# Optimization experiments

Hardware: AMD Instinct MI355X
Metric: run time of the kernel (lower is better)

## Reference

```python
import jax, jax.numpy as jnp
import numpy as np

EMBED = 512
HEADS = 8
HEAD_DIM = EMBED // HEADS


def setup_inputs() -> dict:
    key = jax.random.key(0)
    ks = jax.random.split(key, 11)
    B, S, E = 2, 4096, EMBED
    scale = 1.0 / np.sqrt(E)
    inp = {
        "q": jax.random.normal(ks[0], (B, S, E), dtype=jnp.float32),
        "k": jax.random.normal(ks[1], (B, S, E), dtype=jnp.float32),
        "v": jax.random.normal(ks[2], (B, S, E), dtype=jnp.float32),
        # linear layer params (torch nn.Linear: y = x @ W.T + b)
        "Wq": jax.random.normal(ks[3], (E, E), dtype=jnp.float32) * scale,
        "bq": jnp.zeros((E,), dtype=jnp.float32),
        "Wk": jax.random.normal(ks[4], (E, E), dtype=jnp.float32) * scale,
        "bk": jnp.zeros((E,), dtype=jnp.float32),
        "Wv": jax.random.normal(ks[5], (E, E), dtype=jnp.float32) * scale,
        "bv": jnp.zeros((E,), dtype=jnp.float32),
        "Wo": jax.random.normal(ks[6], (E, E), dtype=jnp.float32) * scale,
        "bo": jnp.zeros((E,), dtype=jnp.float32),
    }
    return inp


def reference(q, k, v, Wq, bq, Wk, bk, Wv, bv, Wo, bo):
    B, Sq, E = q.shape
    Sk = k.shape[1]
    H, D = HEADS, HEAD_DIM
    # projections, split heads: [B, S, H, D]
    qh = (q @ Wq.T + bq).reshape(B, Sq, H, D)
    kh = (k @ Wk.T + bk).reshape(B, Sk, H, D)
    vh = (v @ Wv.T + bv).reshape(B, Sk, H, D)
    # full score matrix [B, H, Sq, Sk]; note: scaled by sqrt(embed_size), matching source
    scores = jnp.einsum('bqhe,bkhe->bhqk', qh, kh) / jnp.sqrt(jnp.float32(E))
    probs = jax.nn.softmax(scores, axis=-1)
    attn = jnp.einsum('bhql,blhd->bqhd', probs, vh)  # [B, Sq, H, D]
    concat = attn.reshape(B, Sq, E)
    return concat @ Wo.T + bo
```

## Files before the change

kernel.cpp:

```cpp
#include <hip/hip_runtime.h>
#include <hip/hip_bf16.h>

#define DEVFN __device__ __forceinline__

typedef __attribute__((ext_vector_type(8))) __bf16 bf16x8;
typedef __attribute__((ext_vector_type(4))) float f32x4;
typedef __attribute__((ext_vector_type(16))) float f32x16;

constexpr int E  = 512;
constexpr int S  = 4096;
constexpr int HD = 64;
constexpr int RT = 8192;

DEVFN unsigned int cvt_pk_bf16(float lo, float hi) {
  unsigned int r;
  asm("v_cvt_pk_bf16_f32 %0, %1, %2" : "=v"(r) : "v"(lo), "v"(hi));
  return r;
}
DEVFN void plswap(unsigned int& a, unsigned int& b) {
  asm("v_permlane32_swap_b32 %0, %1" : "+v"(a), "+v"(b));
}
DEVFN float ex2(float x) { return __builtin_amdgcn_exp2f(x); }

DEVFN unsigned short f2bf(float f) {
  union { float f; unsigned int u; } v; v.f = f;
  unsigned int u = v.u;
  return (unsigned short)((u + 0x7fffu + ((u >> 16) & 1u)) >> 16);
}

DEVFN f32x4 mfma16(bf16x8 a, bf16x8 b, f32x4 c) {
  return __builtin_amdgcn_mfma_f32_16x16x32_bf16(a, b, c, 0, 0, 0);
}
DEVFN f32x16 mfma32(bf16x8 a, bf16x8 b, f32x16 c) {
  return __builtin_amdgcn_mfma_f32_32x32x16_bf16(a, b, c, 0, 0, 0);
}

DEVFN uint4 pk8(const float4& a, const float4& b) {
  uint4 r;
  r.x = cvt_pk_bf16(a.x, a.y); r.y = cvt_pk_bf16(a.z, a.w);
  r.z = cvt_pk_bf16(b.x, b.y); r.w = cvt_pk_bf16(b.z, b.w);
  return r;
}
DEVFN bf16x8 asbf(uint4 u) { union { uint4 a; bf16x8 b; } c; c.a = u; return c.b; }

template<typename TIN, int OMODE>
DEVFN void gemm_body(const TIN* __restrict__ X, const float* __restrict__ W,
                     const float* __restrict__ bias, void* __restrict__ outp,
                     float scale, unsigned short (*Al)[72], unsigned short (*Bl)[72]) {
  const int bid = blockIdx.x;
  const int bm = bid >> 2, bn = bid & 3;
  const int tid = threadIdx.x;
  const int w = tid >> 6, lane = tid & 63;
  const int g = lane >> 4, ln = lane & 15;
  const int wm = w >> 2, wn = w & 3;
  const int r0 = bm * 128, n0 = bn * 128;
  const int srw = tid >> 2, sc0 = (tid & 3) * 16;

  f32x4 acc[4][2] = {};

  float4 af[4];
  uint4  au[2];
  float4 bp[4];

  auto loadA = [&](int k0) {
    if constexpr (sizeof(TIN) == 4) {
      const float* src = (const float*)X + (size_t)(r0 + srw) * E + k0 + sc0;
      #pragma unroll
      for (int i = 0; i < 4; ++i) af[i] = *(const float4*)(src + i * 4);
    } else {
      const unsigned short* src = (const unsigned short*)X + (size_t)(r0 + srw) * E + k0 + sc0;
      #pragma unroll
      for (int i = 0; i < 2; ++i) au[i] = *(const uint4*)(src + i * 8);
    }
  };
  auto loadB = [&](int k0) {
    const float* src = W + (size_t)(n0 + srw) * E + k0 + sc0;
    #pragma unroll
    for (int i = 0; i < 4; ++i) bp[i] = *(const float4*)(src + i * 4);
  };

  loadA(0); loadB(0);

  for (int k0 = 0; k0 < E; k0 += 64) {
    if constexpr (sizeof(TIN) == 4) {
      *(uint4*)&Al[srw][sc0]     = pk8(af[0], af[1]);
      *(uint4*)&Al[srw][sc0 + 8] = pk8(af[2], af[3]);
    } else {
      *(uint4*)&Al[srw][sc0]     = au[0];
      *(uint4*)&Al[srw][sc0 + 8] = au[1];
    }
    *(uint4*)&Bl[srw][sc0]     = pk8(bp[0], bp[1]);
    *(uint4*)&Bl[srw][sc0 + 8] = pk8(bp[2], bp[3]);
    __syncthreads();
    if (k0 + 64 < E) { loadA(k0 + 64); loadB(k0 + 64); }

    __builtin_amdgcn_s_setprio(1);
    #pragma unroll
    for (int kk = 0; kk < 2; ++kk) {
      bf16x8 afr[4], bfr[2];
      #pragma unroll
      for (int i = 0; i < 4; ++i)
        afr[i] = *(const bf16x8*)&Al[wm*64 + i*16 + ln][kk*32 + 8*g];
      #pragma unroll
      for (int j = 0; j < 2; ++j)
        bfr[j] = *(const bf16x8*)&Bl[wn*32 + j*16 + ln][kk*32 + 8*g];
      #pragma unroll
      for (int i = 0; i < 4; ++i)
        #pragma unroll
        for (int j = 0; j < 2; ++j)
          acc[i][j] = mfma16(afr[i], bfr[j], acc[i][j]);
    }
    __builtin_amdgcn_s_setprio(0);
    __syncthreads();
  }

  #pragma unroll
  for (int j = 0; j < 2; ++j) {
    const int gcol = n0 + wn*32 + j*16 + ln;
    const float bv = bias[gcol];
    #pragma unroll
    for (int i = 0; i < 4; ++i) {
      const int gr = r0 + wm*64 + i*16 + 4*g;
      #pragma unroll
      for (int r = 0; r < 4; ++r) {
        const float v = (acc[i][j][r] + bv) * scale;
        if constexpr (OMODE == 1)
          ((float*)outp)[(size_t)(gr + r) * E + gcol] = v;
        else if constexpr (OMODE == 0)
          ((unsigned short*)outp)[(size_t)(gr + r) * E + gcol] = f2bf(v);
        else
          ((unsigned short*)outp)[((size_t)((gr + r) >> 12) * E + gcol) * S + ((gr + r) & (S - 1))] = f2bf(v);
      }
    }
  }
}

__global__ __launch_bounds__(512) void gemm_qkv(const float* __restrict__ q,
    const float* __restrict__ k, const float* __restrict__ v,
    const float* __restrict__ Wq, const float* __restrict__ bq,
    const float* __restrict__ Wk, const float* __restrict__ bk,
    const float* __restrict__ Wv, const float* __restrict__ bv,
    unsigned short* qh, unsigned short* kh, unsigned short* vhT, float qscale) {
  __shared__ unsigned short Al[128][72];
  __shared__ unsigned short Bl[128][72];
  const int y = blockIdx.y;
  if (y == 0)      gemm_body<float, 0>(q, Wq, bq, qh, qscale, Al, Bl);
  else if (y == 1) gemm_body<float, 0>(k, Wk, bk, kh, 1.0f, Al, Bl);
  else             gemm_body<float, 2>(v, Wv, bv, vhT, 1.0f, Al, Bl);
}

__global__ __launch_bounds__(512) void gemm_o(const unsigned short* __restrict__ cc,
    const float* __restrict__ Wo, const float* __restrict__ bo, float* out) {
  __shared__ unsigned short Al[128][72];
  __shared__ unsigned short Bl[128][72];
  gemm_body<unsigned short, 1>(cc, Wo, bo, out, 1.0f, Al, Bl);
}

__global__ __launch_bounds__(256) void attn_fwd(const unsigned short* __restrict__ qh,
                                                const unsigned short* __restrict__ kh,
                                                const unsigned short* __restrict__ vhT,
                                                unsigned short* __restrict__ cc) {
  __shared__ unsigned short K_lds[64][72];
  __shared__ unsigned short V_lds[64][72];

  const int bid = blockIdx.x;
  const int swz = (bid & 7) * 64 + (bid >> 3);
  const int bh = swz >> 5, qt = swz & 31;
  const int b = bh >> 3, h = bh & 7;

  const int tid = threadIdx.x;
  const int w = tid >> 6, lane = tid & 63;
  const int l31 = lane & 31, hi = lane >> 5;

  const unsigned short* qb = qh + (size_t)b * S * E + h * HD;
  const unsigned short* kb = kh + (size_t)b * S * E + h * HD;
  const unsigned short* vb = vhT + ((size_t)b * E + h * HD) * S;
  const int q0 = qt * 128 + w * 32;

  bf16x8 qf[4];
  #pragma unroll
  for (int kf = 0; kf < 4; ++kf)
    qf[kf] = *(const bf16x8*)(qb + (size_t)(q0 + l31) * E + kf*16 + 8*hi);

  f32x16 o0 = {}, o1 = {};
  float ml = -__builtin_inff(), ll = 0.f;

  const int srow = tid >> 2, sc0 = (tid & 3) * 16;
  const unsigned short* kS = kb + (size_t)srow * E + sc0;
  const unsigned short* vS = vb + (size_t)srow * S + sc0;

  uint4 kr0 = *(const uint4*)kS, kr1 = *(const uint4*)(kS + 8);
  uint4 vr0 = *(const uint4*)vS, vr1 = *(const uint4*)(vS + 8);

  for (int it = 0; it < S / 64; ++it) {
    *(uint4*)&K_lds[srow][sc0]     = kr0;
    *(uint4*)&K_lds[srow][sc0 + 8] = kr1;
    *(uint4*)&V_lds[srow][sc0]     = vr0;
    *(uint4*)&V_lds[srow][sc0 + 8] = vr1;
    __syncthreads();

    if (it + 1 < S / 64) {
      const unsigned short* kp = kS + (size_t)(it + 1) * 64 * E;
      const unsigned short* vp = vS + (it + 1) * 64;
      kr0 = *(const uint4*)kp; kr1 = *(const uint4*)(kp + 8);
      vr0 = *(const uint4*)vp; vr1 = *(const uint4*)(vp + 8);
    }

    f32x16 s0 = {}, s1 = {};
    __builtin_amdgcn_s_setprio(1);
    #pragma unroll
    for (int kf = 0; kf < 4; ++kf) {
      bf16x8 ka = *(const bf16x8*)&K_lds[l31]     [kf*16 + 8*hi];
      bf16x8 kc = *(const bf16x8*)&K_lds[32 + l31][kf*16 + 8*hi];
      s0 = mfma32(ka, qf[kf], s0);
      s1 = mfma32(kc, qf[kf], s1);
    }
    __builtin_amdgcn_s_setprio(0);

    float tm = -__builtin_inff();
    #pragma unroll
    for (int r = 0; r < 16; ++r) tm = fmaxf(tm, fmaxf(s0[r], s1[r]));
    tm = fmaxf(tm, __shfl_xor(tm, 32));

    if (!__all(tm <= ml + 8.f)) {
      const float mn = fmaxf(ml, tm);
      const float fr = ex2(ml - mn);
      ml = mn; ll *= fr;
      #pragma unroll
      for (int r = 0; r < 16; ++r) { o0[r] *= fr; o1[r] *= fr; }
    }

    float rs = 0.f;
    #pragma unroll
    for (int r = 0; r < 16; ++r) {
      s0[r] = ex2(s0[r] - ml); rs += s0[r];
      s1[r] = ex2(s1[r] - ml); rs += s1[r];
    }
    rs += __shfl_xor(rs, 32);
    ll += rs;

    unsigned int a0 = cvt_pk_bf16(s0[0],  s0[1]),  a1 = cvt_pk_bf16(s0[2],  s0[3]);
    unsigned int a2 = cvt_pk_bf16(s0[4],  s0[5]),  a3 = cvt_pk_bf16(s0[6],  s0[7]);
    unsigned int a4 = cvt_pk_bf16(s0[8],  s0[9]),  a5 = cvt_pk_bf16(s0[10], s0[11]);
    unsigned int a6 = cvt_pk_bf16(s0[12], s0[13]), a7 = cvt_pk_bf16(s0[14], s0[15]);
    plswap(a0, a2); plswap(a1, a3); plswap(a4, a6); plswap(a5, a7);
    unsigned int c0 = cvt_pk_bf16(s1[0],  s1[1]),  c1 = cvt_pk_bf16(s1[2],  s1[3]);
    unsigned int c2 = cvt_pk_bf16(s1[4],  s1[5]),  c3 = cvt_pk_bf16(s1[6],  s1[7]);
    unsigned int c4 = cvt_pk_bf16(s1[8],  s1[9]),  c5 = cvt_pk_bf16(s1[10], s1[11]);
    unsigned int c6 = cvt_pk_bf16(s1[12], s1[13]), c7 = cvt_pk_bf16(s1[14], s1[15]);
    plswap(c0, c2); plswap(c1, c3); plswap(c4, c6); plswap(c5, c7);
    uint4 pa[4];
    pa[0] = uint4{a0, a1, a2, a3};
    pa[1] = uint4{a4, a5, a6, a7};
    pa[2] = uint4{c0, c1, c2, c3};
    pa[3] = uint4{c4, c5, c6, c7};

    __builtin_amdgcn_s_setprio(1);
    #pragma unroll
    for (int tf = 0; tf < 4; ++tf) {
      bf16x8 va = *(const bf16x8*)&V_lds[l31]     [tf*16 + 8*hi];
      bf16x8 vc = *(const bf16x8*)&V_lds[32 + l31][tf*16 + 8*hi];
      bf16x8 pf = asbf(pa[tf]);
      o0 = mfma32(va, pf, o0);
      o1 = mfma32(vc, pf, o1);
    }
    __builtin_amdgcn_s_setprio(0);
    __syncthreads();
  }

  const float inv = 1.0f / ll;
  const size_t rowb = (size_t)(b * S + q0 + l31) * E + h * HD;
  #pragma unroll
  for (int qd = 0; qd < 4; ++qd) {
    uint2 w0, w1;
    w0.x = cvt_pk_bf16(o0[4*qd]     * inv, o0[4*qd + 1] * inv);
    w0.y = cvt_pk_bf16(o0[4*qd + 2] * inv, o0[4*qd + 3] * inv);
    *(uint2*)&cc[rowb + 8*qd + 4*hi] = w0;
    w1.x = cvt_pk_bf16(o1[4*qd]     * inv, o1[4*qd + 1] * inv);
    w1.y = cvt_pk_bf16(o1[4*qd + 2] * inv, o1[4*qd + 3] * inv);
    *(uint2*)&cc[rowb + 32 + 8*qd + 4*hi] = w1;
  }
}

extern "C" void kernel_launch(void* const* d_in, const int* in_sizes, int n_in,
                              void* d_out, int out_size, void* d_ws, size_t ws_size,
                              hipStream_t stream) {
  const float* q  = (const float*)d_in[0];
  const float* k  = (const float*)d_in[1];
  const float* v  = (const float*)d_in[2];
  const float* Wq = (const float*)d_in[3];
  const float* bq = (const float*)d_in[4];
  const float* Wk = (const float*)d_in[5];
  const float* bk = (const float*)d_in[6];
  const float* Wv = (const float*)d_in[7];
  const float* bv = (const float*)d_in[8];
  const float* Wo = (const float*)d_in[9];
  const float* bo = (const float*)d_in[10];
  float* out = (float*)d_out;

  unsigned short* qh  = (unsigned short*)d_ws;
  unsigned short* kh  = qh + (size_t)RT * E;
  unsigned short* vhT = kh + (size_t)RT * E;
  unsigned short* cc  = vhT + (size_t)RT * E;

  const float qscale = 1.4426950408889634f / 22.62741699796952f;

  gemm_qkv<<<dim3(256, 3), dim3(512), 0, stream>>>(q, k, v, Wq, bq, Wk, bk, Wv, bv,
                                                   qh, kh, vhT, qscale);
  attn_fwd<<<dim3(512), dim3(256), 0, stream>>>(qh, kh, vhT, cc);
  gemm_o<<<dim3(256), dim3(512), 0, stream>>>(cc, Wo, bo, out);
}
```

Baseline: 157.7 us.

## Split attention KV range across two wave groups per block and merge

Measured after the change: 149.4 us. 5.3% less time.

```diff
diff --git a/kernel.cpp b/kernel.cpp
--- a/kernel.cpp
+++ b/kernel.cpp
@@ -156,12 +156,11 @@
   gemm_body<unsigned short, 1>(cc, Wo, bo, out, 1.0f, Al, Bl);
 }
 
-__global__ __launch_bounds__(256) void attn_fwd(const unsigned short* __restrict__ qh,
+__global__ __launch_bounds__(512) void attn_fwd(const unsigned short* __restrict__ qh,
                                                 const unsigned short* __restrict__ kh,
                                                 const unsigned short* __restrict__ vhT,
                                                 unsigned short* __restrict__ cc) {
-  __shared__ unsigned short K_lds[64][72];
-  __shared__ unsigned short V_lds[64][72];
+  __shared__ unsigned short SM[4][64][72];
 
   const int bid = blockIdx.x;
   const int swz = (bid & 7) * 64 + (bid >> 3);
@@ -169,13 +168,18 @@
   const int b = bh >> 3, h = bh & 7;
 
   const int tid = threadIdx.x;
-  const int w = tid >> 6, lane = tid & 63;
+  const int wv = tid >> 6, lane = tid & 63;
+  const int half = wv >> 2, w4 = wv & 3;
   const int l31 = lane & 31, hi = lane >> 5;
+
+  unsigned short (*K_lds)[72] = SM[2*half];
+  unsigned short (*V_lds)[72] = SM[2*half + 1];
 
   const unsigned short* qb = qh + (size_t)b * S * E + h * HD;
   const unsigned short* kb = kh + (size_t)b * S * E + h * HD;
   const unsigned short* vb = vhT + ((size_t)b * E + h * HD) * S;
-  const int q0 = qt * 128 + w * 32;
+  const int q0 = qt * 128 + w4 * 32;
+  const int tbase = half * (S / 2);
 
   bf16x8 qf[4];
   #pragma unroll
@@ -185,21 +189,23 @@
   f32x16 o0 = {}, o1 = {};
   float ml = -__builtin_inff(), ll = 0.f;
 
-  const int srow = tid >> 2, sc0 = (tid & 3) * 16;
-  const unsigned short* kS = kb + (size_t)srow * E + sc0;
-  const unsigned short* vS = vb + (size_t)srow * S + sc0;
+  const int t256 = tid & 255;
+  const int srow = t256 >> 2, sc0 = (t256 & 3) * 16;
+  const unsigned short* kS = kb + (size_t)(tbase + srow) * E + sc0;
+  const unsigned short* vS = vb + (size_t)srow * S + tbase + sc0;
 
   uint4 kr0 = *(const uint4*)kS, kr1 = *(const uint4*)(kS + 8);
   uint4 vr0 = *(const uint4*)vS, vr1 = *(const uint4*)(vS + 8);
 
-  for (int it = 0; it < S / 64; ++it) {
+  constexpr int NIT = S / 2 / 64;
+  for (int it = 0; it < NIT; ++it) {
     *(uint4*)&K_lds[srow][sc0]     = kr0;
     *(uint4*)&K_lds[srow][sc0 + 8] = kr1;
     *(uint4*)&V_lds[srow][sc0]     = vr0;
     *(uint4*)&V_lds[srow][sc0 + 8] = vr1;
     __syncthreads();
 
-    if (it + 1 < S / 64) {
+    if (it + 1 < NIT) {
       const unsigned short* kp = kS + (size_t)(it + 1) * 64 * E;
       const unsigned short* vp = vS + (it + 1) * 64;
       kr0 = *(const uint4*)kp; kr1 = *(const uint4*)(kp + 8);
@@ -268,17 +274,37 @@
     __syncthreads();
   }
 
-  const float inv = 1.0f / ll;
-  const size_t rowb = (size_t)(b * S + q0 + l31) * E + h * HD;
-  #pragma unroll
-  for (int qd = 0; qd < 4; ++qd) {
-    uint2 w0, w1;
-    w0.x = cvt_pk_bf16(o0[4*qd]     * inv, o0[4*qd + 1] * inv);
-    w0.y = cvt_pk_bf16(o0[4*qd + 2] * inv, o0[4*qd + 3] * inv);
-    *(uint2*)&cc[rowb + 8*qd + 4*hi] = w0;
-    w1.x = cvt_pk_bf16(o1[4*qd]     * inv, o1[4*qd + 1] * inv);
-    w1.y = cvt_pk_bf16(o1[4*qd + 2] * inv, o1[4*qd + 3] * inv);
-    *(uint2*)&cc[rowb + 32 + 8*qd + 4*hi] = w1;
+  float* cb = (float*)SM;
+  float* p = cb + (size_t)(w4 * 64 + lane) * 34;
+  if (half) {
+    #pragma unroll
+    for (int r = 0; r < 16; ++r) { p[r] = o0[r]; p[16 + r] = o1[r]; }
+    p[32] = ml; p[33] = ll;
+  }
+  __syncthreads();
+  if (!half) {
+    const float m2 = p[32], l2 = p[33];
+    const float m = fmaxf(ml, m2);
+    const float f1 = ex2(ml - m), f2 = ex2(m2 - m);
+    ll = ll * f1 + l2 * f2;
+    #pragma unroll
+    for (int r = 0; r < 16; ++r) {
+      o0[r] = o0[r] * f1 + p[r] * f2;
+      o1[r] = o1[r] * f1 + p[16 + r] * f2;
+    }
+
+    const float inv = 1.0f / ll;
+    const size_t rowb = (size_t)(b * S + q0 + l31) * E + h * HD;
+    #pragma unroll
+    for (int qd = 0; qd < 4; ++qd) {
+      uint2 w0, w1;
+      w0.x = cvt_pk_bf16(o0[4*qd]     * inv, o0[4*qd + 1] * inv);
+      w0.y = cvt_pk_bf16(o0[4*qd + 2] * inv, o0[4*qd + 3] * inv);
+      *(uint2*)&cc[rowb + 8*qd + 4*hi] = w0;
+      w1.x = cvt_pk_bf16(o1[4*qd]     * inv, o1[4*qd + 1] * inv);
+      w1.y = cvt_pk_bf16(o1[4*qd + 2] * inv, o1[4*qd + 3] * inv);
+      *(uint2*)&cc[rowb + 32 + 8*qd + 4*hi] = w1;
+    }
   }
 }
 
@@ -307,6 +333,6 @@
 
   gemm_qkv<<<dim3(256, 3), dim3(512), 0, stream>>>(q, k, v, Wq, bq, Wk, bk, Wv, bv,
                                                    qh, kh, vhT, qscale);
-  attn_fwd<<<dim3(512), dim3(256), 0, stream>>>(qh, kh, vhT, cc);
+  attn_fwd<<<dim3(512), dim3(512), 0, stream>>>(qh, kh, vhT, cc);
   gemm_o<<<dim3(256), dim3(512), 0, stream>>>(cc, Wo, bo, out);
 }
```
